# Kernel optimization log

Measured on AMD Instinct MI355X. Metric: run time of the kernel, lower is better.

## Reference

```python
import jax, jax.numpy as jnp
import numpy as np
import math

HEAD = 4
D_MODEL = 128
N_NODES = 2048
SEQ_LEN = 1
D_K = D_MODEL // HEAD
BATCH = 64


def conv1x1_relu(x, w, b):
    # x: [B, C, N, L], w: [O, C], b: [O]  (1x1 Conv2d + ReLU; dropout is identity in eval)
    return jax.nn.relu(jnp.einsum('oc,bcnl->bonl', w, x) + b[None, :, None, None])


def setup_inputs() -> dict:
    key = jax.random.key(0)
    ks = jax.random.split(key, 12)
    s = 0.05
    return {
        'x': jax.random.normal(ks[0], (BATCH, D_MODEL, N_NODES, SEQ_LEN), jnp.float32),
        'q_w': jax.random.normal(ks[1], (D_MODEL, D_MODEL), jnp.float32) * s,
        'q_b': jnp.zeros((D_MODEL,), jnp.float32),
        'v_w': jax.random.normal(ks[2], (D_MODEL, D_MODEL), jnp.float32) * s,
        'v_b': jnp.zeros((D_MODEL,), jnp.float32),
        'c_w': jax.random.normal(ks[3], (D_MODEL, D_MODEL), jnp.float32) * s,
        'c_b': jnp.zeros((D_MODEL,), jnp.float32),
        'memory': jax.random.normal(ks[4], (HEAD, SEQ_LEN, N_NODES, D_K), jnp.float32) * s,
        'nodevec1': jax.random.normal(ks[5], (N_NODES, 10), jnp.float32),
        'nodevec2': jax.random.normal(ks[6], (10, N_NODES), jnp.float32),
        'weights_pool': jax.random.normal(ks[7], (SEQ_LEN, 3, 3), jnp.float32) * s,
        'bias_pool': jax.random.normal(ks[8], (N_NODES, D_K), jnp.float32) * s,
        'aff_w': jnp.ones((D_MODEL, N_NODES, SEQ_LEN), jnp.float32),
        'aff_b': jnp.zeros((D_MODEL, N_NODES, SEQ_LEN), jnp.float32),
    }


def reference(x, q_w, q_b, v_w, v_b, c_w, c_b, memory, nodevec1, nodevec2,
              weights_pool, bias_pool, aff_w, aff_b):
    B = x.shape[0]
    scale = math.sqrt(D_K)

    query = conv1x1_relu(x, q_w, q_b)
    value = conv1x1_relu(x, v_w, v_b)

    # [B, d_model, N, L] -> [B, h, d_k, N, L] -> [B, h, L, N, d_k]
    def split_heads(t):
        return t.reshape(B, HEAD, D_K, N_NODES, SEQ_LEN).transpose(0, 1, 4, 3, 2)

    query = split_heads(query)
    value = split_heads(value)

    key_ = jax.nn.softmax(memory / scale, axis=-1)      # [h, L, N, d_k]
    query = jax.nn.softmax(query / scale, axis=-1)      # [B, h, L, N, d_k]

    Aapt = jax.nn.softmax(jax.nn.relu(nodevec1 @ nodevec2), axis=-1)  # [N, N]

    kv = jnp.einsum('hlnx,bhlny->bhlxy', key_, value)          # [B,h,L,d_k,d_k]
    attn_qkv = jnp.einsum('bhlnx,bhlxy->bhlny', query, kv)     # [B,h,L,N,d_k]

    weights = jnp.einsum('nm,dio->nio', Aapt, weights_pool)    # [N,3,3]
    bias_dyn = Aapt @ bias_pool                                # [N,d_k]
    attn_dyn = jnp.einsum('bhlnc,nio->bhlnc', value, weights) + bias_dyn[None, None, None, :, :]

    out = attn_qkv + attn_dyn                                  # [B,h,L,N,d_k]
    out = out.transpose(0, 1, 4, 3, 2).reshape(B, D_MODEL, N_NODES, SEQ_LEN)
    out = conv1x1_relu(out, c_w, c_b)

    # num_nodes (2048) not in [170, 358, 5] -> affine-residual branch runs
    out = out * aff_w[None] + aff_b[None] + out
    return out
```

## Files before the change

### kernel.cpp

```cpp
#include <hip/hip_runtime.h>

#define NB 64
#define CH 128
#define NNODE 2048
#define NH 4
#define DKK 32
#define INVS 0.17677669529663687f

typedef __bf16 bf16x8 __attribute__((ext_vector_type(8)));
typedef float f32x4 __attribute__((ext_vector_type(4)));
typedef unsigned short ushort_t;

union U16x8 { uint4 u; bf16x8 b; unsigned short s[8]; };
union U16x4 { uint2 u; unsigned short s[4]; };

__device__ inline bf16x8 as_bf16x8(uint4 u){ U16x8 x; x.u = u; return x.b; }
__device__ inline unsigned short f2b(float f){ __bf16 h = (__bf16)f; return __builtin_bit_cast(unsigned short, h); }
__device__ inline float b2f(unsigned short u){ __bf16 h = __builtin_bit_cast(__bf16, u); return (float)h; }

#define XT_IDX(n, c) ((n) * 136 + ((c) ^ ((((n) >> 2) & 7) << 3)))

__global__ __launch_bounds__(256) void k0_prep(const float* __restrict__ qw,
    const float* __restrict__ vw, const float* __restrict__ cw,
    const float* __restrict__ memory, const float* __restrict__ bias_pool,
    ushort_t* __restrict__ wqb, ushort_t* __restrict__ wvb, ushort_t* __restrict__ wcb,
    ushort_t* __restrict__ keysT, float* __restrict__ bias_dyn,
    ushort_t* __restrict__ bpT)
{
  int gid = blockIdx.x * 256 + threadIdx.x;
  if (gid < 16384) { wqb[gid] = f2b(qw[gid]); wvb[gid] = f2b(vw[gid]); wcb[gid] = f2b(cw[gid]); }
  bias_dyn[gid] = 0.f;
  { int k = gid >> 11, m = gid & 2047;
    bpT[gid] = f2b(bias_pool[m * 32 + k]); }
  if (gid < 8192) {
    int h = gid >> 11, n = gid & 2047;
    const float* src = memory + (size_t)gid * 32;
    float v[32]; float m = -1e30f;
    #pragma unroll
    for (int i = 0; i < 32; ++i) { v[i] = src[i] * INVS; m = fmaxf(m, v[i]); }
    float s = 0.f;
    #pragma unroll
    for (int i = 0; i < 32; ++i) { v[i] = __expf(v[i] - m); s += v[i]; }
    float inv = 1.f / s;
    #pragma unroll
    for (int i = 0; i < 32; ++i)
      keysT[(size_t)(h * 32 + i) * 2048 + n] = f2b(v[i] * inv);
  }
}

__global__ __launch_bounds__(256) void kb1(const float* __restrict__ nv1,
    const float* __restrict__ nv2, ushort_t* __restrict__ Ebuf)
{
  int n = blockIdx.x; int tid = threadIdx.x;
  float a1[10];
  #pragma unroll
  for (int d = 0; d < 10; ++d) a1[d] = nv1[n * 10 + d];
  int m0 = tid * 8;
  float s[8];
  #pragma unroll
  for (int j = 0; j < 8; ++j) s[j] = 0.f;
  #pragma unroll
  for (int d = 0; d < 10; ++d) {
    const float* p = nv2 + d * 2048 + m0;
    float4 u = *(const float4*)p; float4 v = *(const float4*)(p + 4);
    s[0] += a1[d] * u.x; s[1] += a1[d] * u.y; s[2] += a1[d] * u.z; s[3] += a1[d] * u.w;
    s[4] += a1[d] * v.x; s[5] += a1[d] * v.y; s[6] += a1[d] * v.z; s[7] += a1[d] * v.w;
  }
  float e[8]; float sum = 0.f;
  #pragma unroll
  for (int j = 0; j < 8; ++j) { e[j] = __expf(fmaxf(s[j], 0.f)); sum += e[j]; }
  #pragma unroll
  for (int d = 1; d < 64; d <<= 1) sum += __shfl_xor(sum, d);
  __shared__ float red[4];
  if ((tid & 63) == 0) red[tid >> 6] = sum;
  __syncthreads();
  float inv = 1.f / (red[0] + red[1] + red[2] + red[3]);
  U16x8 o;
  #pragma unroll
  for (int j = 0; j < 8; ++j) o.s[j] = f2b(e[j] * inv);
  *(uint4*)(Ebuf + (size_t)n * 2048 + m0) = o.u;
}

__global__ __launch_bounds__(256) void kb2(const ushort_t* __restrict__ Ebuf,
    const ushort_t* __restrict__ bpT, float* __restrict__ bias_dyn)
{
  int bid = blockIdx.x;
  int n0 = (bid >> 3) * 128;
  int m0 = (bid & 7) * 256;
  int tid = threadIdx.x; int wv = tid >> 6; int lane = tid & 63;
  int quad = lane >> 4; int l16 = lane & 15;
  int r0 = n0 + 32 * wv;
  f32x4 zero4 = {0.f,0.f,0.f,0.f};
  f32x4 acc[2][2];
  acc[0][0] = zero4; acc[0][1] = zero4; acc[1][0] = zero4; acc[1][1] = zero4;
  for (int ks = 0; ks < 256; ks += 32) {
    int mb = m0 + ks + 8 * quad;
    bf16x8 a0 = *(const bf16x8*)(Ebuf + (size_t)(r0 + l16) * 2048 + mb);
    bf16x8 a1 = *(const bf16x8*)(Ebuf + (size_t)(r0 + 16 + l16) * 2048 + mb);
    bf16x8 b0 = *(const bf16x8*)(bpT + (size_t)l16 * 2048 + mb);
    bf16x8 b1 = *(const bf16x8*)(bpT + (size_t)(16 + l16) * 2048 + mb);
    acc[0][0] = __builtin_amdgcn_mfma_f32_16x16x32_bf16(a0, b0, acc[0][0], 0, 0, 0);
    acc[0][1] = __builtin_amdgcn_mfma_f32_16x16x32_bf16(a0, b1, acc[0][1], 0, 0, 0);
    acc[1][0] = __builtin_amdgcn_mfma_f32_16x16x32_bf16(a1, b0, acc[1][0], 0, 0, 0);
    acc[1][1] = __builtin_amdgcn_mfma_f32_16x16x32_bf16(a1, b1, acc[1][1], 0, 0, 0);
  }
  #pragma unroll
  for (int rt = 0; rt < 2; ++rt)
    #pragma unroll
    for (int ct = 0; ct < 2; ++ct)
      #pragma unroll
      for (int r = 0; r < 4; ++r)
        atomicAdd(bias_dyn + (size_t)(r0 + 16*rt + 4*quad + r) * 32 + 16*ct + l16,
                  acc[rt][ct][r]);
}

__global__ __launch_bounds__(256, 4) void k1_qv(const float* __restrict__ x,
    const ushort_t* __restrict__ wqb, const ushort_t* __restrict__ wvb,
    const float* __restrict__ qbias, const float* __restrict__ vbias,
    const ushort_t* __restrict__ keysT,
    ushort_t* __restrict__ QsT, ushort_t* __restrict__ VT,
    float* __restrict__ kvp)
{
  int bid = blockIdx.x; int b = bid >> 5; int n0 = (bid & 31) * 64;
  int tid = threadIdx.x; int wv = tid >> 6; int lane = tid & 63;
  int quad = lane >> 4; int l16 = lane & 15;
  __shared__ __align__(16) ushort_t XT[64 * 136];
  __shared__ __align__(16) ushort_t QO[64][136];

  f32x4 zero4 = {0.f,0.f,0.f,0.f};

  uint4 wq[2][4];
  #pragma unroll
  for (int ct = 0; ct < 2; ++ct)
    #pragma unroll
    for (int k0 = 0; k0 < 4; ++k0)
      wq[ct][k0] = *(const uint4*)(wqb + (32 * wv + 16 * ct + l16) * 128 + 32 * k0 + 8 * quad);

  #pragma unroll
  for (int p = 0; p < 2; ++p) {
    int c4 = 4 * ((tid >> 4) + 16 * p);
    int n4 = 4 * (tid & 15);
    float4 r[4];
    #pragma unroll
    for (int j = 0; j < 4; ++j)
      r[j] = *(const float4*)(x + (size_t)(b * 128 + c4 + j) * 2048 + n0 + n4);
    #pragma unroll
    for (int i = 0; i < 4; ++i) {
      U16x4 w;
      w.s[0] = f2b(((const float*)&r[0])[i]);
      w.s[1] = f2b(((const float*)&r[1])[i]);
      w.s[2] = f2b(((const float*)&r[2])[i]);
      w.s[3] = f2b(((const float*)&r[3])[i]);
      *(uint2*)&XT[XT_IDX(n4 + i, c4)] = w.u;
    }
  }
  __syncthreads();

  {
    float4 qb4[2];
    #pragma unroll
    for (int ct = 0; ct < 2; ++ct)
      qb4[ct] = *(const float4*)(qbias + 32 * wv + 16 * ct + 4 * quad);
    #pragma unroll
    for (int nt = 0; nt < 4; ++nt) {
      f32x4 aq[2]; aq[0] = zero4; aq[1] = zero4;
      #pragma unroll
      for (int k0 = 0; k0 < 4; ++k0) {
        bf16x8 bfrag = *(const bf16x8*)&XT[XT_IDX(16 * nt + l16, 32 * k0 + 8 * quad)];
        aq[0] = __builtin_amdgcn_mfma_f32_16x16x32_bf16(as_bf16x8(wq[0][k0]), bfrag, aq[0], 0, 0, 0);
        aq[1] = __builtin_amdgcn_mfma_f32_16x16x32_bf16(as_bf16x8(wq[1][k0]), bfrag, aq[1], 0, 0, 0);
      }
      float sq[2][4]; float mx = -1e30f;
      #pragma unroll
      for (int ct = 0; ct < 2; ++ct)
        #pragma unroll
        for (int r = 0; r < 4; ++r) {
          sq[ct][r] = fmaxf(aq[ct][r] + ((const float*)&qb4[ct])[r], 0.f) * INVS;
          mx = fmaxf(mx, sq[ct][r]);
        }
      mx = fmaxf(mx, __shfl_xor(mx, 16));
      mx = fmaxf(mx, __shfl_xor(mx, 32));
      float sum = 0.f;
      #pragma unroll
      for (int ct = 0; ct < 2; ++ct)
        #pragma unroll
        for (int r = 0; r < 4; ++r) { sq[ct][r] = __expf(sq[ct][r] - mx); sum += sq[ct][r]; }
      sum += __shfl_xor(sum, 16);
      sum += __shfl_xor(sum, 32);
      float inv = 1.f / sum;
      #pragma unroll
      for (int ct = 0; ct < 2; ++ct) {
        U16x4 w;
        #pragma unroll
        for (int r = 0; r < 4; ++r) w.s[r] = f2b(sq[ct][r] * inv);
        *(uint2*)&QO[16 * nt + l16][32 * wv + 16 * ct + 4 * quad] = w.u;
      }
    }
  }

  uint2 vout[4][2];
  {
    uint4 wvw[2][4];
    #pragma unroll
    for (int ct = 0; ct < 2; ++ct)
      #pragma unroll
      for (int k0 = 0; k0 < 4; ++k0)
        wvw[ct][k0] = *(const uint4*)(wvb + (32 * wv + 16 * ct + l16) * 128 + 32 * k0 + 8 * quad);
    float4 vb4[2];
    #pragma unroll
    for (int ct = 0; ct < 2; ++ct)
      vb4[ct] = *(const float4*)(vbias + 32 * wv + 16 * ct + 4 * quad);
    #pragma unroll
    for (int nt = 0; nt < 4; ++nt) {
      f32x4 av[2]; av[0] = zero4; av[1] = zero4;
      #pragma unroll
      for (int k0 = 0; k0 < 4; ++k0) {
        bf16x8 bfrag = *(const bf16x8*)&XT[XT_IDX(16 * nt + l16, 32 * k0 + 8 * quad)];
        av[0] = __builtin_amdgcn_mfma_f32_16x16x32_bf16(as_bf16x8(wvw[0][k0]), bfrag, av[0], 0, 0, 0);
        av[1] = __builtin_amdgcn_mfma_f32_16x16x32_bf16(as_bf16x8(wvw[1][k0]), bfrag, av[1], 0, 0, 0);
      }
      #pragma unroll
      for (int ct = 0; ct < 2; ++ct) {
        U16x4 w;
        #pragma unroll
        for (int r = 0; r < 4; ++r)
          w.s[r] = f2b(fmaxf(av[ct][r] + ((const float*)&vb4[ct])[r], 0.f));
        vout[nt][ct] = w.u;
      }
    }
  }
  __syncthreads();

  #pragma unroll
  for (int nt = 0; nt < 4; ++nt)
    #pragma unroll
    for (int ct = 0; ct < 2; ++ct)
      *(uint2*)&XT[XT_IDX(16 * nt + l16, 32 * wv + 16 * ct + 4 * quad)] = vout[nt][ct];
  __syncthreads();

  {
    f32x4 akv[2][2];
    akv[0][0] = zero4; akv[0][1] = zero4; akv[1][0] = zero4; akv[1][1] = zero4;
    #pragma unroll
    for (int ks = 0; ks < 2; ++ks) {
      const ushort_t* kp = keysT + (size_t)(32 * wv) * 2048 + n0 + 32 * ks + 8 * quad;
      bf16x8 ka0 = *(const bf16x8*)(kp + (size_t)l16 * 2048);
      bf16x8 ka1 = *(const bf16x8*)(kp + (size_t)(16 + l16) * 2048);
      U16x8 v0, v1;
      #pragma unroll
      for (int j = 0; j < 8; ++j) {
        int rowk = 32 * ks + 8 * quad + j;
        v0.s[j] = XT[XT_IDX(rowk, 32 * wv + l16)];
        v1.s[j] = XT[XT_IDX(rowk, 32 * wv + 16 + l16)];
      }
      akv[0][0] = __builtin_amdgcn_mfma_f32_16x16x32_bf16(ka0, v0.b, akv[0][0], 0, 0, 0);
      akv[0][1] = __builtin_amdgcn_mfma_f32_16x16x32_bf16(ka0, v1.b, akv[0][1], 0, 0, 0);
      akv[1][0] = __builtin_amdgcn_mfma_f32_16x16x32_bf16(ka1, v0.b, akv[1][0], 0, 0, 0);
      akv[1][1] = __builtin_amdgcn_mfma_f32_16x16x32_bf16(ka1, v1.b, akv[1][1], 0, 0, 0);
    }
    float* kdst = kvp + (size_t)bid * 4096 + wv * 1024;
    #pragma unroll
    for (int xt = 0; xt < 2; ++xt)
      #pragma unroll
      for (int yt = 0; yt < 2; ++yt)
        #pragma unroll
        for (int r = 0; r < 4; ++r)
          kdst[(16 * yt + l16) * 32 + 16 * xt + 4 * quad + r] = akv[xt][yt][r];
  }

  #pragma unroll
  for (int j = 0; j < 4; ++j) {
    int id = tid + 256 * j; int n = id >> 4; int u = id & 15;
    size_t go = (size_t)(b * 2048 + n0 + n) * 128 + 8 * u;
    *(uint4*)(QsT + go) = *(uint4*)&QO[n][8 * u];
    *(uint4*)(VT  + go) = *(uint4*)&XT[XT_IDX(n, 8 * u)];
  }
}

__global__ __launch_bounds__(256) void kred(const float* __restrict__ kvp,
    float* __restrict__ kvws)
{
  int gid = blockIdx.x * 256 + threadIdx.x;
  int b = gid >> 10; int i = gid & 1023;
  const float* p = kvp + (size_t)(b * 32) * 4096 + i * 4;
  float4 s = {0.f,0.f,0.f,0.f};
  #pragma unroll
  for (int t = 0; t < 32; ++t) {
    float4 v = *(const float4*)(p + (size_t)t * 4096);
    s.x += v.x; s.y += v.y; s.z += v.z; s.w += v.w;
  }
  *(float4*)(kvws + (size_t)gid * 4) = s;
}

__global__ __launch_bounds__(256, 3) void k3_out(const ushort_t* __restrict__ QsT,
    const ushort_t* __restrict__ VT, const float* __restrict__ kvws,
    const float* __restrict__ bias_dyn, const ushort_t* __restrict__ wcb,
    const float* __restrict__ cbias, const float* __restrict__ wpool,
    const float* __restrict__ aff_w, const float* __restrict__ aff_b,
    float* __restrict__ out)
{
  int bid = blockIdx.x; int b = bid >> 5; int n0 = (bid & 31) * 64;
  int tid = threadIdx.x; int wv = tid >> 6; int lane = tid & 63;
  int quad = lane >> 4; int l16 = lane & 15;
  __shared__ __align__(16) char smem[53760];
  ushort_t (*kvT)[32][40] = (ushort_t(*)[32][40])(smem);
  ushort_t (*MID)[136]    = (ushort_t(*)[136])(smem + 10240);
  ushort_t (*VL)[132]     = (ushort_t(*)[132])(smem + 27648);
  float    (*BD)[36]      = (float(*)[36])(smem + 44544);
  float    (*OST)[64]     = (float(*)[64])(smem + 10240);

  float Ws = 0.f;
  #pragma unroll
  for (int i = 0; i < 9; ++i) Ws += wpool[i];

  uint4 wc[2][4];
  #pragma unroll
  for (int mt = 0; mt < 2; ++mt)
    #pragma unroll
    for (int k0 = 0; k0 < 4; ++k0)
      wc[mt][k0] = *(const uint4*)(wcb + (32 * wv + 16 * mt + l16) * 128 + 32 * k0 + 8 * quad);

  #pragma unroll
  for (int p = 0; p < 16; ++p) {
    int id = tid + 256 * p;
    kvT[id >> 10][(id >> 5) & 31][id & 31] = f2b(kvws[(size_t)b * 4096 + id]);
  }
  #pragma unroll
  for (int p = 0; p < 4; ++p) {
    int id = tid + 256 * p; int n = id >> 4; int u = id & 15;
    *(uint4*)&VL[n][8 * u] = *(const uint4*)(VT + (size_t)(b * 2048 + n0 + n) * 128 + 8 * u);
  }
  #pragma unroll
  for (int p = 0; p < 2; ++p) {
    int id = tid + 256 * p; int n = id >> 3; int g = id & 7;
    *(float4*)&BD[n][4 * g] = *(const float4*)(bias_dyn + (size_t)(n0 + n) * 32 + 4 * g);
  }
  __syncthreads();

  f32x4 zero4 = {0.f,0.f,0.f,0.f};
  f32x4 acc1[4][2];
  #pragma unroll
  for (int nt = 0; nt < 4; ++nt) { acc1[nt][0] = zero4; acc1[nt][1] = zero4; }
  #pragma unroll
  for (int nt = 0; nt < 4; ++nt) {
    bf16x8 aq = *(const bf16x8*)(QsT + (size_t)(b * 2048 + n0 + 16 * nt + l16) * 128 + 32 * wv + 8 * quad);
    #pragma unroll
    for (int ct = 0; ct < 2; ++ct)
      acc1[nt][ct] = __builtin_amdgcn_mfma_f32_16x16x32_bf16(
          aq, *(const bf16x8*)&kvT[wv][16 * ct + l16][8 * quad], acc1[nt][ct], 0, 0, 0);
  }

  #pragma unroll
  for (int nt = 0; nt < 4; ++nt)
    #pragma unroll
    for (int ct = 0; ct < 2; ++ct)
      #pragma unroll
      for (int r = 0; r < 4; ++r) {
        int nl = 16 * nt + 4 * quad + r;
        int cc = 32 * wv + 16 * ct + l16;
        float v = b2f(VL[nl][cc]);
        float bd = BD[nl][16 * ct + l16];
        MID[nl][cc] = f2b(acc1[nt][ct][r] + Ws * v + bd);
      }
  __syncthreads();

  f32x4 acc2[2][4];
  #pragma unroll
  for (int mt = 0; mt < 2; ++mt)
    #pragma unroll
    for (int nt = 0; nt < 4; ++nt) acc2[mt][nt] = zero4;
  #pragma unroll
  for (int k0 = 0; k0 < 4; ++k0) {
    bf16x8 bb[4];
    #pragma unroll
    for (int nt = 0; nt < 4; ++nt)
      bb[nt] = *(const bf16x8*)&MID[16 * nt + l16][32 * k0 + 8 * quad];
    #pragma unroll
    for (int mt = 0; mt < 2; ++mt)
      #pragma unroll
      for (int nt = 0; nt < 4; ++nt)
        acc2[mt][nt] = __builtin_amdgcn_mfma_f32_16x16x32_bf16(
            as_bf16x8(wc[mt][k0]), bb[nt], acc2[mt][nt], 0, 0, 0);
  }
  __syncthreads();

  float4 cb4[2];
  #pragma unroll
  for (int mt = 0; mt < 2; ++mt)
    cb4[mt] = *(const float4*)(cbias + 32 * wv + 16 * mt + 4 * quad);
  #pragma unroll
  for (int mt = 0; mt < 2; ++mt)
    #pragma unroll
    for (int nt = 0; nt < 4; ++nt)
      #pragma unroll
      for (int r = 0; r < 4; ++r) {
        int c_out = 32 * wv + 16 * mt + 4 * quad + r;
        OST[c_out][16 * nt + l16] = fmaxf(acc2[mt][nt][r] + ((const float*)&cb4[mt])[r], 0.f);
      }
  __syncthreads();

  #pragma unroll
  for (int p = 0; p < 8; ++p) {
    int id = tid + 256 * p; int c = id >> 4; int g = id & 15;
    float4 y = *(const float4*)&OST[c][4 * g];
    size_t ai = (size_t)c * 2048 + n0 + 4 * g;
    float4 aw4 = *(const float4*)(aff_w + ai);
    float4 ab4 = *(const float4*)(aff_b + ai);
    float4 o;
    o.x = y.x * aw4.x + ab4.x + y.x;
    o.y = y.y * aw4.y + ab4.y + y.y;
    o.z = y.z * aw4.z + ab4.z + y.z;
    o.w = y.w * aw4.w + ab4.w + y.w;
    *(float4*)(out + (size_t)(b * 128 + c) * 2048 + n0 + 4 * g) = o;
  }
}

extern "C" void kernel_launch(void* const* d_in, const int* in_sizes, int n_in,
                              void* d_out, int out_size, void* d_ws, size_t ws_size,
                              hipStream_t stream)
{
  const float* x      = (const float*)d_in[0];
  const float* qw     = (const float*)d_in[1];
  const float* qb     = (const float*)d_in[2];
  const float* vw     = (const float*)d_in[3];
  const float* vb     = (const float*)d_in[4];
  const float* cw     = (const float*)d_in[5];
  const float* cb     = (const float*)d_in[6];
  const float* memory = (const float*)d_in[7];
  const float* nv1    = (const float*)d_in[8];
  const float* nv2    = (const float*)d_in[9];
  const float* wpool  = (const float*)d_in[10];
  const float* bpool  = (const float*)d_in[11];
  const float* aw     = (const float*)d_in[12];
  const float* ab     = (const float*)d_in[13];
  float* out = (float*)d_out;

  char* ws = (char*)d_ws;
  ushort_t* QsT      = (ushort_t*)(ws);
  ushort_t* VT       = (ushort_t*)(ws + 33554432);
  float*    kvws     = (float*)   (ws + 67108864);
  ushort_t* keysT    = (ushort_t*)(ws + 68157440);
  float*    bias_dyn = (float*)   (ws + 69206016);
  ushort_t* wqb      = (ushort_t*)(ws + 69468160);
  ushort_t* wvb      = (ushort_t*)(ws + 69500928);
  ushort_t* wcb      = (ushort_t*)(ws + 69533696);
  ushort_t* Ebuf     = (ushort_t*)(ws + 69566464);
  ushort_t* bpT      = (ushort_t*)(ws + 77955072);
  float*    kvp      = (float*)   (ws + 78086144);

  k0_prep<<<256, 256, 0, stream>>>(qw, vw, cw, memory, bpool, wqb, wvb, wcb,
                                   keysT, bias_dyn, bpT);
  kb1<<<2048, 256, 0, stream>>>(nv1, nv2, Ebuf);
  kb2<<<128, 256, 0, stream>>>(Ebuf, bpT, bias_dyn);
  k1_qv<<<2048, 256, 0, stream>>>(x, wqb, wvb, qb, vb, keysT, QsT, VT, kvp);
  kred<<<256, 256, 0, stream>>>(kvp, kvws);
  k3_out<<<2048, 256, 0, stream>>>(QsT, VT, kvws, bias_dyn, wcb, cb, wpool, aw, ab, out);
}
```

Measured before the change: 215.9 us.

## Merge prep kernels into two launches, batch x loads, drop softmax max pass

Combines k0_prep with kb1 into one launch, and kb2 with k1_qv into another, using block-index ranges to pick the role. This cuts the launch count from six to four and lets independent work run side by side. All x loads in k1 are now issued before any conversion, which gives more memory-level parallelism. The query softmax no longer subtracts the row max, since the inputs are ReLU outputs scaled down. That removes two shuffles and a pass, at the cost of possible overflow if the activations are large.

```diff
diff --git a/kernel.cpp b/kernel.cpp
--- a/kernel.cpp
+++ b/kernel.cpp
@@ -20,114 +20,114 @@
 
 #define XT_IDX(n, c) ((n) * 136 + ((c) ^ ((((n) >> 2) & 7) << 3)))
 
-__global__ __launch_bounds__(256) void k0_prep(const float* __restrict__ qw,
+__global__ __launch_bounds__(256) void kA(const float* __restrict__ qw,
     const float* __restrict__ vw, const float* __restrict__ cw,
     const float* __restrict__ memory, const float* __restrict__ bias_pool,
     ushort_t* __restrict__ wqb, ushort_t* __restrict__ wvb, ushort_t* __restrict__ wcb,
     ushort_t* __restrict__ keysT, float* __restrict__ bias_dyn,
-    ushort_t* __restrict__ bpT)
+    ushort_t* __restrict__ bpT,
+    const float* __restrict__ nv1, const float* __restrict__ nv2,
+    ushort_t* __restrict__ Ebuf)
 {
-  int gid = blockIdx.x * 256 + threadIdx.x;
-  if (gid < 16384) { wqb[gid] = f2b(qw[gid]); wvb[gid] = f2b(vw[gid]); wcb[gid] = f2b(cw[gid]); }
-  bias_dyn[gid] = 0.f;
-  { int k = gid >> 11, m = gid & 2047;
-    bpT[gid] = f2b(bias_pool[m * 32 + k]); }
-  if (gid < 8192) {
-    int h = gid >> 11, n = gid & 2047;
-    const float* src = memory + (size_t)gid * 32;
-    float v[32]; float m = -1e30f;
-    #pragma unroll
-    for (int i = 0; i < 32; ++i) { v[i] = src[i] * INVS; m = fmaxf(m, v[i]); }
-    float s = 0.f;
-    #pragma unroll
-    for (int i = 0; i < 32; ++i) { v[i] = __expf(v[i] - m); s += v[i]; }
-    float inv = 1.f / s;
-    #pragma unroll
-    for (int i = 0; i < 32; ++i)
-      keysT[(size_t)(h * 32 + i) * 2048 + n] = f2b(v[i] * inv);
+  __shared__ float red[4];
+  int tid = threadIdx.x;
+  if (blockIdx.x < 256) {
+    int gid = blockIdx.x * 256 + tid;
+    if (gid < 16384) { wqb[gid] = f2b(qw[gid]); wvb[gid] = f2b(vw[gid]); wcb[gid] = f2b(cw[gid]); }
+    bias_dyn[gid] = 0.f;
+    { int k = gid >> 11, m = gid & 2047;
+      bpT[gid] = f2b(bias_pool[m * 32 + k]); }
+    if (gid < 8192) {
+      int h = gid >> 11, n = gid & 2047;
+      const float* src = memory + (size_t)gid * 32;
+      float v[32]; float m = -1e30f;
+      #pragma unroll
+      for (int i = 0; i < 32; ++i) { v[i] = src[i] * INVS; m = fmaxf(m, v[i]); }
+      float s = 0.f;
+      #pragma unroll
+      for (int i = 0; i < 32; ++i) { v[i] = __expf(v[i] - m); s += v[i]; }
+      float inv = 1.f / s;
+      #pragma unroll
+      for (int i = 0; i < 32; ++i)
+        keysT[(size_t)(h * 32 + i) * 2048 + n] = f2b(v[i] * inv);
+    }
+  } else {
+    int n = blockIdx.x - 256;
+    float a1[10];
+    #pragma unroll
+    for (int d = 0; d < 10; ++d) a1[d] = nv1[n * 10 + d];
+    int m0 = tid * 8;
+    float s[8];
+    #pragma unroll
+    for (int j = 0; j < 8; ++j) s[j] = 0.f;
+    #pragma unroll
+    for (int d = 0; d < 10; ++d) {
+      const float* p = nv2 + d * 2048 + m0;
+      float4 u = *(const float4*)p; float4 v = *(const float4*)(p + 4);
+      s[0] += a1[d] * u.x; s[1] += a1[d] * u.y; s[2] += a1[d] * u.z; s[3] += a1[d] * u.w;
+      s[4] += a1[d] * v.x; s[5] += a1[d] * v.y; s[6] += a1[d] * v.z; s[7] += a1[d] * v.w;
+    }
+    float e[8]; float sum = 0.f;
+    #pragma unroll
+    for (int j = 0; j < 8; ++j) { e[j] = __expf(fmaxf(s[j], 0.f)); sum += e[j]; }
+    #pragma unroll
+    for (int d = 1; d < 64; d <<= 1) sum += __shfl_xor(sum, d);
+    if ((tid & 63) == 0) red[tid >> 6] = sum;
+    __syncthreads();
+    float inv = 1.f / (red[0] + red[1] + red[2] + red[3]);
+    U16x8 o;
+    #pragma unroll
+    for (int j = 0; j < 8; ++j) o.s[j] = f2b(e[j] * inv);
+    *(uint4*)(Ebuf + (size_t)n * 2048 + m0) = o.u;
   }
 }
 
-__global__ __launch_bounds__(256) void kb1(const float* __restrict__ nv1,
-    const float* __restrict__ nv2, ushort_t* __restrict__ Ebuf)
-{
-  int n = blockIdx.x; int tid = threadIdx.x;
-  float a1[10];
-  #pragma unroll
-  for (int d = 0; d < 10; ++d) a1[d] = nv1[n * 10 + d];
-  int m0 = tid * 8;
-  float s[8];
-  #pragma unroll
-  for (int j = 0; j < 8; ++j) s[j] = 0.f;
-  #pragma unroll
-  for (int d = 0; d < 10; ++d) {
-    const float* p = nv2 + d * 2048 + m0;
-    float4 u = *(const float4*)p; float4 v = *(const float4*)(p + 4);
-    s[0] += a1[d] * u.x; s[1] += a1[d] * u.y; s[2] += a1[d] * u.z; s[3] += a1[d] * u.w;
-    s[4] += a1[d] * v.x; s[5] += a1[d] * v.y; s[6] += a1[d] * v.z; s[7] += a1[d] * v.w;
-  }
-  float e[8]; float sum = 0.f;
-  #pragma unroll
-  for (int j = 0; j < 8; ++j) { e[j] = __expf(fmaxf(s[j], 0.f)); sum += e[j]; }
-  #pragma unroll
-  for (int d = 1; d < 64; d <<= 1) sum += __shfl_xor(sum, d);
-  __shared__ float red[4];
-  if ((tid & 63) == 0) red[tid >> 6] = sum;
-  __syncthreads();
-  float inv = 1.f / (red[0] + red[1] + red[2] + red[3]);
-  U16x8 o;
-  #pragma unroll
-  for (int j = 0; j < 8; ++j) o.s[j] = f2b(e[j] * inv);
-  *(uint4*)(Ebuf + (size_t)n * 2048 + m0) = o.u;
-}
-
-__global__ __launch_bounds__(256) void kb2(const ushort_t* __restrict__ Ebuf,
-    const ushort_t* __restrict__ bpT, float* __restrict__ bias_dyn)
-{
-  int bid = blockIdx.x;
-  int n0 = (bid >> 3) * 128;
-  int m0 = (bid & 7) * 256;
-  int tid = threadIdx.x; int wv = tid >> 6; int lane = tid & 63;
-  int quad = lane >> 4; int l16 = lane & 15;
-  int r0 = n0 + 32 * wv;
-  f32x4 zero4 = {0.f,0.f,0.f,0.f};
-  f32x4 acc[2][2];
-  acc[0][0] = zero4; acc[0][1] = zero4; acc[1][0] = zero4; acc[1][1] = zero4;
-  for (int ks = 0; ks < 256; ks += 32) {
-    int mb = m0 + ks + 8 * quad;
-    bf16x8 a0 = *(const bf16x8*)(Ebuf + (size_t)(r0 + l16) * 2048 + mb);
-    bf16x8 a1 = *(const bf16x8*)(Ebuf + (size_t)(r0 + 16 + l16) * 2048 + mb);
-    bf16x8 b0 = *(const bf16x8*)(bpT + (size_t)l16 * 2048 + mb);
-    bf16x8 b1 = *(const bf16x8*)(bpT + (size_t)(16 + l16) * 2048 + mb);
-    acc[0][0] = __builtin_amdgcn_mfma_f32_16x16x32_bf16(a0, b0, acc[0][0], 0, 0, 0);
-    acc[0][1] = __builtin_amdgcn_mfma_f32_16x16x32_bf16(a0, b1, acc[0][1], 0, 0, 0);
-    acc[1][0] = __builtin_amdgcn_mfma_f32_16x16x32_bf16(a1, b0, acc[1][0], 0, 0, 0);
-    acc[1][1] = __builtin_amdgcn_mfma_f32_16x16x32_bf16(a1, b1, acc[1][1], 0, 0, 0);
-  }
-  #pragma unroll
-  for (int rt = 0; rt < 2; ++rt)
-    #pragma unroll
-    for (int ct = 0; ct < 2; ++ct)
-      #pragma unroll
-      for (int r = 0; r < 4; ++r)
-        atomicAdd(bias_dyn + (size_t)(r0 + 16*rt + 4*quad + r) * 32 + 16*ct + l16,
-                  acc[rt][ct][r]);
-}
-
-__global__ __launch_bounds__(256, 4) void k1_qv(const float* __restrict__ x,
+__global__ __launch_bounds__(256, 4) void kB(
+    const ushort_t* __restrict__ Ebuf, const ushort_t* __restrict__ bpT,
+    float* __restrict__ bias_dyn,
+    const float* __restrict__ x,
     const ushort_t* __restrict__ wqb, const ushort_t* __restrict__ wvb,
     const float* __restrict__ qbias, const float* __restrict__ vbias,
     const ushort_t* __restrict__ keysT,
     ushort_t* __restrict__ QsT, ushort_t* __restrict__ VT,
     float* __restrict__ kvp)
 {
-  int bid = blockIdx.x; int b = bid >> 5; int n0 = (bid & 31) * 64;
+  __shared__ __align__(16) ushort_t XT[64 * 136];
+  __shared__ __align__(16) ushort_t QO[64][136];
   int tid = threadIdx.x; int wv = tid >> 6; int lane = tid & 63;
   int quad = lane >> 4; int l16 = lane & 15;
-  __shared__ __align__(16) ushort_t XT[64 * 136];
-  __shared__ __align__(16) ushort_t QO[64][136];
-
   f32x4 zero4 = {0.f,0.f,0.f,0.f};
+
+  if (blockIdx.x < 128) {
+    int bid = blockIdx.x;
+    int n0 = (bid >> 3) * 128;
+    int m0 = (bid & 7) * 256;
+    int r0 = n0 + 32 * wv;
+    f32x4 acc[2][2];
+    acc[0][0] = zero4; acc[0][1] = zero4; acc[1][0] = zero4; acc[1][1] = zero4;
+    for (int ks = 0; ks < 256; ks += 32) {
+      int mb = m0 + ks + 8 * quad;
+      bf16x8 a0 = *(const bf16x8*)(Ebuf + (size_t)(r0 + l16) * 2048 + mb);
+      bf16x8 a1 = *(const bf16x8*)(Ebuf + (size_t)(r0 + 16 + l16) * 2048 + mb);
+      bf16x8 b0 = *(const bf16x8*)(bpT + (size_t)l16 * 2048 + mb);
+      bf16x8 b1 = *(const bf16x8*)(bpT + (size_t)(16 + l16) * 2048 + mb);
+      acc[0][0] = __builtin_amdgcn_mfma_f32_16x16x32_bf16(a0, b0, acc[0][0], 0, 0, 0);
+      acc[0][1] = __builtin_amdgcn_mfma_f32_16x16x32_bf16(a0, b1, acc[0][1], 0, 0, 0);
+      acc[1][0] = __builtin_amdgcn_mfma_f32_16x16x32_bf16(a1, b0, acc[1][0], 0, 0, 0);
+      acc[1][1] = __builtin_amdgcn_mfma_f32_16x16x32_bf16(a1, b1, acc[1][1], 0, 0, 0);
+    }
+    #pragma unroll
+    for (int rt = 0; rt < 2; ++rt)
+      #pragma unroll
+      for (int ct = 0; ct < 2; ++ct)
+        #pragma unroll
+        for (int r = 0; r < 4; ++r)
+          atomicAdd(bias_dyn + (size_t)(r0 + 16*rt + 4*quad + r) * 32 + 16*ct + l16,
+                    acc[rt][ct][r]);
+    return;
+  }
+
+  int bid = blockIdx.x - 128; int b = bid >> 5; int n0 = (bid & 31) * 64;
 
   uint4 wq[2][4];
   #pragma unroll
@@ -136,22 +136,28 @@
     for (int k0 = 0; k0 < 4; ++k0)
       wq[ct][k0] = *(const uint4*)(wqb + (32 * wv + 16 * ct + l16) * 128 + 32 * k0 + 8 * quad);
 
-  #pragma unroll
-  for (int p = 0; p < 2; ++p) {
-    int c4 = 4 * ((tid >> 4) + 16 * p);
+  {
+    float4 r[8];
     int n4 = 4 * (tid & 15);
-    float4 r[4];
-    #pragma unroll
-    for (int j = 0; j < 4; ++j)
-      r[j] = *(const float4*)(x + (size_t)(b * 128 + c4 + j) * 2048 + n0 + n4);
-    #pragma unroll
-    for (int i = 0; i < 4; ++i) {
-      U16x4 w;
-      w.s[0] = f2b(((const float*)&r[0])[i]);
-      w.s[1] = f2b(((const float*)&r[1])[i]);
-      w.s[2] = f2b(((const float*)&r[2])[i]);
-      w.s[3] = f2b(((const float*)&r[3])[i]);
-      *(uint2*)&XT[XT_IDX(n4 + i, c4)] = w.u;
+    #pragma unroll
+    for (int p = 0; p < 2; ++p) {
+      int c4 = 4 * ((tid >> 4) + 16 * p);
+      #pragma unroll
+      for (int j = 0; j < 4; ++j)
+        r[4 * p + j] = *(const float4*)(x + (size_t)(b * 128 + c4 + j) * 2048 + n0 + n4);
+    }
+    #pragma unroll
+    for (int p = 0; p < 2; ++p) {
+      int c4 = 4 * ((tid >> 4) + 16 * p);
+      #pragma unroll
+      for (int i = 0; i < 4; ++i) {
+        U16x4 w;
+        w.s[0] = f2b(((const float*)&r[4 * p + 0])[i]);
+        w.s[1] = f2b(((const float*)&r[4 * p + 1])[i]);
+        w.s[2] = f2b(((const float*)&r[4 * p + 2])[i]);
+        w.s[3] = f2b(((const float*)&r[4 * p + 3])[i]);
+        *(uint2*)&XT[XT_IDX(n4 + i, c4)] = w.u;
+      }
     }
   }
   __syncthreads();
@@ -170,21 +176,14 @@
         aq[0] = __builtin_amdgcn_mfma_f32_16x16x32_bf16(as_bf16x8(wq[0][k0]), bfrag, aq[0], 0, 0, 0);
         aq[1] = __builtin_amdgcn_mfma_f32_16x16x32_bf16(as_bf16x8(wq[1][k0]), bfrag, aq[1], 0, 0, 0);
       }
-      float sq[2][4]; float mx = -1e30f;
+      float sq[2][4]; float sum = 0.f;
       #pragma unroll
       for (int ct = 0; ct < 2; ++ct)
         #pragma unroll
         for (int r = 0; r < 4; ++r) {
-          sq[ct][r] = fmaxf(aq[ct][r] + ((const float*)&qb4[ct])[r], 0.f) * INVS;
-          mx = fmaxf(mx, sq[ct][r]);
+          sq[ct][r] = __expf(fmaxf(aq[ct][r] + ((const float*)&qb4[ct])[r], 0.f) * INVS);
+          sum += sq[ct][r];
         }
-      mx = fmaxf(mx, __shfl_xor(mx, 16));
-      mx = fmaxf(mx, __shfl_xor(mx, 32));
-      float sum = 0.f;
-      #pragma unroll
-      for (int ct = 0; ct < 2; ++ct)
-        #pragma unroll
-        for (int r = 0; r < 4; ++r) { sq[ct][r] = __expf(sq[ct][r] - mx); sum += sq[ct][r]; }
       sum += __shfl_xor(sum, 16);
       sum += __shfl_xor(sum, 32);
       float inv = 1.f / sum;
@@ -448,11 +447,10 @@
   ushort_t* bpT      = (ushort_t*)(ws + 77955072);
   float*    kvp      = (float*)   (ws + 78086144);
 
-  k0_prep<<<256, 256, 0, stream>>>(qw, vw, cw, memory, bpool, wqb, wvb, wcb,
-                                   keysT, bias_dyn, bpT);
-  kb1<<<2048, 256, 0, stream>>>(nv1, nv2, Ebuf);
-  kb2<<<128, 256, 0, stream>>>(Ebuf, bpT, bias_dyn);
-  k1_qv<<<2048, 256, 0, stream>>>(x, wqb, wvb, qb, vb, keysT, QsT, VT, kvp);
+  kA<<<2304, 256, 0, stream>>>(qw, vw, cw, memory, bpool, wqb, wvb, wcb,
+                               keysT, bias_dyn, bpT, nv1, nv2, Ebuf);
+  kB<<<2176, 256, 0, stream>>>(Ebuf, bpT, bias_dyn, x, wqb, wvb, qb, vb,
+                               keysT, QsT, VT, kvp);
   kred<<<256, 256, 0, stream>>>(kvp, kvws);
   k3_out<<<2048, 256, 0, stream>>>(QsT, VT, kvws, bias_dyn, wcb, cb, wpool, aw, ab, out);
 }
```

After: 209.0 us. 3.2% less time.
